# Kernel optimization log

Measured on AMD Instinct MI355X. Metric: run time of the kernel, lower is better.

## Reference

```python
import jax, jax.numpy as jnp
import numpy as np

ALPHA = 0.1
LAMBDA_1 = 10.0
LAMBDA_2 = 0.1
GAMMA = 0.1
MAX_RANK = 32  # rank loss only uses first min(B, 32) samples


def setup_inputs() -> dict:
    key = jax.random.key(0)
    k1, k2 = jax.random.split(key)
    B, d = 4096, 64
    Lambda_pred = jax.random.normal(k1, (B, d, d), dtype=jnp.float32)
    Lambda_true = jax.random.normal(k2, (B, d, d), dtype=jnp.float32)
    return {"Lambda_pred": Lambda_pred, "Lambda_true": Lambda_true}


def reference(Lambda_pred, Lambda_true):
    # L_efficiency: mean squared error over all entries
    efficiency_loss = jnp.mean((Lambda_pred - Lambda_true) ** 2)

    # traces of each (d, d) matrix -> shape (B,)
    tr_pred = jnp.diagonal(Lambda_pred, axis1=-2, axis2=-1).sum(-1)
    tr_true = jnp.diagonal(Lambda_true, axis1=-2, axis2=-1).sum(-1)

    B = tr_pred.shape[0]
    m = min(B, MAX_RANK)  # static
    if B > 1:
        p = tr_pred[:m]
        t = tr_true[:m]
        # pairwise diffs, shape (m, m): entry [i, j] = x_i - x_j
        dt = t[:, None] - t[None, :]
        dp = p[:, None] - p[None, :]
        # if t_i > t_j: relu(p_j - p_i + gamma); elif t_j > t_i: relu(p_i - p_j + gamma); else 0
        contrib = jnp.where(
            dt > 0,
            jax.nn.relu(-dp + GAMMA),
            jnp.where(dt < 0, jax.nn.relu(dp + GAMMA), 0.0),
        )
        upper = jnp.triu(jnp.ones((m, m), dtype=contrib.dtype), k=1)  # i < j pairs
        n_pairs = m * (m - 1) // 2
        rank_loss = jnp.sum(contrib * upper) / max(n_pairs, 1)
    else:
        rank_loss = jnp.asarray(0.0, dtype=efficiency_loss.dtype)

    total = efficiency_loss + LAMBDA_2 * rank_loss
    return total, efficiency_loss, rank_loss
```

## Files before the change

### kernel.cpp

```cpp
#include <hip/hip_runtime.h>

#define BATCH   4096
#define DIM     64
#define NTOT    (BATCH * DIM * DIM)
#define NVEC    (NTOT / 4)
#define MRANK   32
#define GAMMA_C   0.1f
#define LAMBDA2_C 0.1f

#define THREADS 256
#define BLOCKS  2048
#define STRIDE  (BLOCKS * THREADS)
#define ITERS   (NVEC / STRIDE)

__global__ void __launch_bounds__(THREADS, 2)
partial_sumsq_kernel(const float4* __restrict__ p, const float4* __restrict__ t,
                     float* __restrict__ partials) {
    const int tid = blockIdx.x * THREADS + threadIdx.x;

    float4 a[ITERS], b[ITERS];
    #pragma unroll
    for (int k = 0; k < ITERS; ++k) a[k] = p[tid + k * STRIDE];
    #pragma unroll
    for (int k = 0; k < ITERS; ++k) b[k] = t[tid + k * STRIDE];

    float acc = 0.0f;
    #pragma unroll
    for (int k = 0; k < ITERS; ++k) {
        float dx = a[k].x - b[k].x;
        float dy = a[k].y - b[k].y;
        float dz = a[k].z - b[k].z;
        float dw = a[k].w - b[k].w;
        acc += dx * dx + dy * dy + dz * dz + dw * dw;
    }

    #pragma unroll
    for (int off = 32; off > 0; off >>= 1)
        acc += __shfl_down(acc, off, 64);

    __shared__ float smem[THREADS / 64];
    const int wid  = threadIdx.x >> 6;
    const int lane = threadIdx.x & 63;
    if (lane == 0) smem[wid] = acc;
    __syncthreads();
    if (threadIdx.x == 0)
        partials[blockIdx.x] = smem[0] + smem[1] + smem[2] + smem[3];
}

__global__ void __launch_bounds__(THREADS)
finish_kernel(const float* __restrict__ p, const float* __restrict__ t,
              const float* __restrict__ partials, float* __restrict__ out) {
    const int tid = threadIdx.x;

    float s = 0.0f;
    #pragma unroll
    for (int k = 0; k < BLOCKS / THREADS; ++k)
        s += partials[tid + k * THREADS];

    const int mat  = tid >> 3;
    const int part = tid & 7;
    float tp = 0.0f, tr = 0.0f;
    #pragma unroll
    for (int i = 0; i < 8; ++i) {
        const int j = part * 8 + i;
        const size_t off = (size_t)mat * (DIM * DIM) + (size_t)j * (DIM + 1);
        tp += p[off];
        tr += t[off];
    }

    #pragma unroll
    for (int off = 32; off > 0; off >>= 1)
        s += __shfl_down(s, off, 64);
    __shared__ float smem[THREADS / 64];
    const int wid  = tid >> 6;
    const int lane = tid & 63;
    if (lane == 0) smem[wid] = s;

    __shared__ float redp[THREADS], redt[THREADS];
    redp[tid] = tp;
    redt[tid] = tr;
    __syncthreads();

    __shared__ float sp[MRANK], st[MRANK];
    if (tid < MRANK) {
        float s1 = 0.0f, s2 = 0.0f;
        #pragma unroll
        for (int i = 0; i < 8; ++i) {
            s1 += redp[tid * 8 + i];
            s2 += redt[tid * 8 + i];
        }
        sp[tid] = s1;
        st[tid] = s2;
    }
    __syncthreads();

    float racc = 0.0f;
    if (tid < MRANK) {
        const float pi = sp[tid];
        const float ti = st[tid];
        for (int j = tid + 1; j < MRANK; ++j) {
            float dt = ti - st[j];
            float dp = pi - sp[j];
            float c = 0.0f;
            if (dt > 0.0f)      c = fmaxf(-dp + GAMMA_C, 0.0f);
            else if (dt < 0.0f) c = fmaxf( dp + GAMMA_C, 0.0f);
            racc += c;
        }
    }
    if (tid < 64) {
        #pragma unroll
        for (int off = 32; off > 0; off >>= 1)
            racc += __shfl_down(racc, off, 64);
        if (tid == 0) {
            float total_ss = smem[0] + smem[1] + smem[2] + smem[3];
            float eff  = total_ss / (float)NTOT;
            float rank = racc / 496.0f;
            out[0] = eff + LAMBDA2_C * rank;
            out[1] = eff;
            out[2] = rank;
        }
    }
}

extern "C" void kernel_launch(void* const* d_in, const int* in_sizes, int n_in,
                              void* d_out, int out_size, void* d_ws, size_t ws_size,
                              hipStream_t stream) {
    const float* pred = (const float*)d_in[0];
    const float* tru  = (const float*)d_in[1];
    float* out = (float*)d_out;
    float* ws  = (float*)d_ws;

    partial_sumsq_kernel<<<BLOCKS, THREADS, 0, stream>>>(
        (const float4*)pred, (const float4*)tru, ws);

    finish_kernel<<<1, THREADS, 0, stream>>>(pred, tru, ws, out);
}
```

Baseline: 155.2 us.

## Fuse partial and finish kernels with last-block atomic counter reduction

```diff
diff --git a/kernel.cpp b/kernel.cpp
--- a/kernel.cpp
+++ b/kernel.cpp
@@ -9,88 +9,105 @@
 #define LAMBDA2_C 0.1f
 
 #define THREADS 256
-#define BLOCKS  2048
-#define STRIDE  (BLOCKS * THREADS)
+#define SBLOCKS 4096
+#define GRID    (SBLOCKS + 1)
+#define STRIDE  (SBLOCKS * THREADS)
 #define ITERS   (NVEC / STRIDE)
 
-__global__ void __launch_bounds__(THREADS, 2)
-partial_sumsq_kernel(const float4* __restrict__ p, const float4* __restrict__ t,
-                     float* __restrict__ partials) {
-    const int tid = blockIdx.x * THREADS + threadIdx.x;
 
-    float4 a[ITERS], b[ITERS];
-    #pragma unroll
-    for (int k = 0; k < ITERS; ++k) a[k] = p[tid + k * STRIDE];
-    #pragma unroll
-    for (int k = 0; k < ITERS; ++k) b[k] = t[tid + k * STRIDE];
+__global__ void __launch_bounds__(THREADS, 4)
+fused_loss_kernel(const float* __restrict__ pred, const float* __restrict__ tru,
+                  float* __restrict__ ws, float* __restrict__ out)
+{
+    const int tid = threadIdx.x;
+    const int bid = blockIdx.x;
 
-    float acc = 0.0f;
-    #pragma unroll
-    for (int k = 0; k < ITERS; ++k) {
-        float dx = a[k].x - b[k].x;
-        float dy = a[k].y - b[k].y;
-        float dz = a[k].z - b[k].z;
-        float dw = a[k].w - b[k].w;
-        acc += dx * dx + dy * dy + dz * dz + dw * dw;
+    float* partials = ws;
+    float* trp = ws + SBLOCKS;
+    float* trt = ws + SBLOCKS + MRANK;
+    unsigned int* cnt = (unsigned int*)(ws + SBLOCKS + 2 * MRANK);
+
+    __shared__ float smem[THREADS / 64];
+    __shared__ float red[2][THREADS];
+    __shared__ float sp[MRANK], st[MRANK];
+    __shared__ int   is_last;
+
+    if (bid == 0) {
+        const int mat  = tid >> 3;
+        const int part = tid & 7;
+        float tp = 0.0f, tr = 0.0f;
+        #pragma unroll
+        for (int i = 0; i < 8; ++i) {
+            const int j = part * 8 + i;
+            const size_t off = (size_t)mat * (DIM * DIM) + (size_t)j * (DIM + 1);
+            tp += pred[off];
+            tr += tru[off];
+        }
+        red[0][tid] = tp;
+        red[1][tid] = tr;
+        __syncthreads();
+        if (tid < MRANK) {
+            float s1 = 0.0f, s2 = 0.0f;
+            #pragma unroll
+            for (int i = 0; i < 8; ++i) {
+                s1 += red[0][tid * 8 + i];
+                s2 += red[1][tid * 8 + i];
+            }
+            __hip_atomic_store(&trp[tid], s1, __ATOMIC_RELAXED, __HIP_MEMORY_SCOPE_AGENT);
+            __hip_atomic_store(&trt[tid], s2, __ATOMIC_RELAXED, __HIP_MEMORY_SCOPE_AGENT);
+        }
+    } else {
+        const int g = (bid - 1) * THREADS + tid;
+        const float4* __restrict__ p4 = (const float4*)pred;
+        const float4* __restrict__ t4 = (const float4*)tru;
+        float4 a[ITERS], b[ITERS];
+        #pragma unroll
+        for (int k = 0; k < ITERS; ++k) a[k] = p4[g + k * STRIDE];
+        #pragma unroll
+        for (int k = 0; k < ITERS; ++k) b[k] = t4[g + k * STRIDE];
+
+        float acc = 0.0f;
+        #pragma unroll
+        for (int k = 0; k < ITERS; ++k) {
+            const float dx = a[k].x - b[k].x;
+            const float dy = a[k].y - b[k].y;
+            const float dz = a[k].z - b[k].z;
+            const float dw = a[k].w - b[k].w;
+            acc += dx * dx + dy * dy + dz * dz + dw * dw;
+        }
+        #pragma unroll
+        for (int off = 32; off > 0; off >>= 1)
+            acc += __shfl_down(acc, off, 64);
+        if ((tid & 63) == 0) smem[tid >> 6] = acc;
+        __syncthreads();
+        if (tid == 0)
+            __hip_atomic_store(&partials[bid - 1],
+                               smem[0] + smem[1] + smem[2] + smem[3],
+                               __ATOMIC_RELAXED, __HIP_MEMORY_SCOPE_AGENT);
     }
 
-    #pragma unroll
-    for (int off = 32; off > 0; off >>= 1)
-        acc += __shfl_down(acc, off, 64);
+    __syncthreads();
+    if (tid == 0) {
+        __threadfence();
+        const unsigned int old = atomicAdd(cnt, 1u);
+        is_last = (old == (unsigned int)(GRID - 1)) ? 1 : 0;
+    }
+    __syncthreads();
+    if (!is_last) return;
 
-    __shared__ float smem[THREADS / 64];
-    const int wid  = threadIdx.x >> 6;
-    const int lane = threadIdx.x & 63;
-    if (lane == 0) smem[wid] = acc;
-    __syncthreads();
-    if (threadIdx.x == 0)
-        partials[blockIdx.x] = smem[0] + smem[1] + smem[2] + smem[3];
-}
-
-__global__ void __launch_bounds__(THREADS)
-finish_kernel(const float* __restrict__ p, const float* __restrict__ t,
-              const float* __restrict__ partials, float* __restrict__ out) {
-    const int tid = threadIdx.x;
-
+    __threadfence();
     float s = 0.0f;
     #pragma unroll
-    for (int k = 0; k < BLOCKS / THREADS; ++k)
-        s += partials[tid + k * THREADS];
-
-    const int mat  = tid >> 3;
-    const int part = tid & 7;
-    float tp = 0.0f, tr = 0.0f;
-    #pragma unroll
-    for (int i = 0; i < 8; ++i) {
-        const int j = part * 8 + i;
-        const size_t off = (size_t)mat * (DIM * DIM) + (size_t)j * (DIM + 1);
-        tp += p[off];
-        tr += t[off];
-    }
-
+    for (int k = 0; k < SBLOCKS / THREADS; ++k)
+        s += __hip_atomic_load(&partials[tid + k * THREADS],
+                               __ATOMIC_RELAXED, __HIP_MEMORY_SCOPE_AGENT);
     #pragma unroll
     for (int off = 32; off > 0; off >>= 1)
         s += __shfl_down(s, off, 64);
-    __shared__ float smem[THREADS / 64];
-    const int wid  = tid >> 6;
-    const int lane = tid & 63;
-    if (lane == 0) smem[wid] = s;
-
-    __shared__ float redp[THREADS], redt[THREADS];
-    redp[tid] = tp;
-    redt[tid] = tr;
-    __syncthreads();
-
-    __shared__ float sp[MRANK], st[MRANK];
+    if ((tid & 63) == 0) smem[tid >> 6] = s;
     if (tid < MRANK) {
-        float s1 = 0.0f, s2 = 0.0f;
-        #pragma unroll
-        for (int i = 0; i < 8; ++i) {
-            s1 += redp[tid * 8 + i];
-            s2 += redt[tid * 8 + i];
-        }
-        sp[tid] = s1;
-        st[tid] = s2;
+        sp[tid] = __hip_atomic_load(&trp[tid], __ATOMIC_RELAXED, __HIP_MEMORY_SCOPE_AGENT);
+        st[tid] = __hip_atomic_load(&trt[tid], __ATOMIC_RELAXED, __HIP_MEMORY_SCOPE_AGENT);
     }
     __syncthreads();
 
@@ -98,13 +115,16 @@
     if (tid < MRANK) {
         const float pi = sp[tid];
         const float ti = st[tid];
-        for (int j = tid + 1; j < MRANK; ++j) {
-            float dt = ti - st[j];
-            float dp = pi - sp[j];
-            float c = 0.0f;
-            if (dt > 0.0f)      c = fmaxf(-dp + GAMMA_C, 0.0f);
-            else if (dt < 0.0f) c = fmaxf( dp + GAMMA_C, 0.0f);
-            racc += c;
+        #pragma unroll
+        for (int j = 0; j < MRANK; ++j) {
+            if (j > tid) {
+                const float dt = ti - st[j];
+                const float dp = pi - sp[j];
+                float c = 0.0f;
+                if (dt > 0.0f)      c = fmaxf(-dp + GAMMA_C, 0.0f);
+                else if (dt < 0.0f) c = fmaxf( dp + GAMMA_C, 0.0f);
+                racc += c;
+            }
         }
     }
     if (tid < 64) {
@@ -112,9 +132,9 @@
         for (int off = 32; off > 0; off >>= 1)
             racc += __shfl_down(racc, off, 64);
         if (tid == 0) {
-            float total_ss = smem[0] + smem[1] + smem[2] + smem[3];
-            float eff  = total_ss / (float)NTOT;
-            float rank = racc / 496.0f;
+            const float total_ss = smem[0] + smem[1] + smem[2] + smem[3];
+            const float eff  = total_ss / (float)NTOT;
+            const float rank = racc / 496.0f;
             out[0] = eff + LAMBDA2_C * rank;
             out[1] = eff;
             out[2] = rank;
@@ -130,8 +150,8 @@
     float* out = (float*)d_out;
     float* ws  = (float*)d_ws;
 
-    partial_sumsq_kernel<<<BLOCKS, THREADS, 0, stream>>>(
-        (const float4*)pred, (const float4*)tru, ws);
+    unsigned int* cnt = (unsigned int*)(ws + SBLOCKS + 2 * MRANK);
+    hipMemsetAsync(cnt, 0, sizeof(unsigned int), stream);
 
-    finish_kernel<<<1, THREADS, 0, stream>>>(pred, tru, ws, out);
+    fused_loss_kernel<<<GRID, THREADS, 0, stream>>>(pred, tru, ws, out);
 }
```

After: 340.8 us. 120% more time.
